# Kernel tuning notes

Measured on AMD Instinct MI355X. Metric: run time of the kernel, lower is better.

## Reference

```python
import jax, jax.numpy as jnp
import numpy as np

B, N, C = 8, 4096, 1024
H = 16
D = C // H  # head_dim = 64
SCALE = D ** -0.5


def setup_inputs() -> dict:
    key = jax.random.key(0)
    ks = jax.random.split(key, 5)
    std = C ** -0.5
    return {
        "x": jax.random.normal(ks[0], (B, N, C), dtype=jnp.float32),
        "Wq": jax.random.normal(ks[1], (C, C), dtype=jnp.float32) * std,
        "Wk": jax.random.normal(ks[2], (C, C), dtype=jnp.float32) * std,
        "Wv": jax.random.normal(ks[3], (C, C), dtype=jnp.float32) * std,
        "Wo": jax.random.normal(ks[4], (C, C), dtype=jnp.float32) * std,
        "bo": jnp.zeros((C,), dtype=jnp.float32),
    }


def reference(x, Wq, Wk, Wv, Wo, bo):
    b, n, c = x.shape
    # projections -> (B, N, H, D)
    q = (x @ Wq).reshape(b, n, H, D)
    k = (x @ Wk).reshape(b, n, H, D)
    v = (x @ Wv).reshape(b, n, H, D)
    # feature maps: softmax over head_dim for q, over sequence for k
    q = jax.nn.softmax(q, axis=-1) * SCALE
    k = jax.nn.softmax(k, axis=1)
    # O(N) linear attention: kv summary then apply to q
    kv = jnp.einsum("bnhf,bnhd->bhfd", k, v)   # (B, H, D, D)
    y = jnp.einsum("bnhf,bhfd->bnhd", q, kv)   # (B, N, H, D)
    y = y.reshape(b, n, H * D)
    return y @ Wo + bo
```

## Files before the change

kernel.cpp:

```cpp
#include <hip/hip_runtime.h>


typedef unsigned short u16;
typedef __bf16 bf16x8v __attribute__((ext_vector_type(8)));
typedef float f32x4 __attribute__((ext_vector_type(4)));
typedef u16 u16x8 __attribute__((ext_vector_type(8)));
typedef u16 u16x4 __attribute__((ext_vector_type(4)));

#define AS1C(p) (const __attribute__((address_space(1))) void*)(p)
#define AS3(p)  (__attribute__((address_space(3))) void*)(p)

__device__ __forceinline__ float b2f(u16 u) {
    union { unsigned u; float f; } c; c.u = ((unsigned)u) << 16; return c.f;
}
__device__ __forceinline__ u16 f2b(float f) {
    union { float f; unsigned u; } c; c.f = f;
    unsigned x = c.u + 0x7fffu + ((c.u >> 16) & 1u);
    return (u16)(x >> 16);
}

__global__ void cast_x_kernel(const float* __restrict__ in, u16* __restrict__ out, long n4) {
    long i = (long)blockIdx.x * blockDim.x + threadIdx.x;
    long stride = (long)gridDim.x * blockDim.x;
    for (long j = i; j < n4; j += stride) {
        float4 v = ((const float4*)in)[j];
        u16x4 o = { f2b(v.x), f2b(v.y), f2b(v.z), f2b(v.w) };
        ((u16x4*)out)[j] = o;
    }
}

__global__ void transpose_cast4(const float* __restrict__ Wq, const float* __restrict__ Wk,
                                const float* __restrict__ Wv, const float* __restrict__ Wo,
                                u16* __restrict__ wt, u16* __restrict__ wot) {
    __shared__ float tl[64][65];
    const int which = blockIdx.x >> 8;
    const float* src = which == 0 ? Wq : which == 1 ? Wk : which == 2 ? Wv : Wo;
    u16* dst = which < 3 ? wt + which * 1048576 : wot;
    const int bx = blockIdx.x & 255;
    const int tx = bx & 15, ty = bx >> 4;
    const int j = threadIdx.x & 63, i0 = threadIdx.x >> 6;
    #pragma unroll
    for (int it = 0; it < 16; ++it) {
        int i = it * 4 + i0;
        tl[i][j] = src[(ty * 64 + i) * 1024 + tx * 64 + j];
    }
    __syncthreads();
    #pragma unroll
    for (int it = 0; it < 16; ++it) {
        int i = it * 4 + i0;
        dst[(tx * 64 + i) * 1024 + ty * 64 + j] = f2b(tl[j][i]);
    }
}

template<int OUTMODE>
__global__ __launch_bounds__(512, 2) void gemm256(
    const u16* __restrict__ A, const u16* __restrict__ Bt,
    void* __restrict__ Cout, const float* __restrict__ bias,
    const int lda, const int ldc, const int ntn, const int nwg)
{
    __shared__ __align__(16) u16 lds[65536];
    const int t = threadIdx.x;
    const int w = t >> 6, lane = t & 63;
    const int l16 = lane & 15, g = lane >> 4;
    const int wr = w >> 2, wc = w & 3;

    const int cpx = nwg >> 3;
    const int bid = blockIdx.x;
    const int swzb = (bid & 7) * cpx + (bid >> 3);
    const int tm = swzb / ntn, tn = swzb - tm * ntn;
    const long row0 = (long)tm << 8, col0 = (long)tn << 8;

    const int rloc = (w << 3) + (lane >> 3);
    const int eo = (((lane & 7) ^ (lane >> 3)) << 3);
    const u16* pA = A + (row0 + rloc) * (long)lda + eo;
    const u16* pB = Bt + (col0 + rloc) * 1024L + eo;
    const long a64 = (long)lda << 6;
    const int wdst = w << 9;

#define STG_A(Tt, j) __builtin_amdgcn_global_load_lds(                        \
    AS1C(pA + (long)(j) * a64 + ((long)(Tt) << 6)),                           \
    AS3(lds + ((((Tt) & 1) << 15) + ((j) << 12) + wdst)), 16, 0, 0);
#define STG_B(Tt, j) __builtin_amdgcn_global_load_lds(                        \
    AS1C(pB + (long)(j) * 65536L + ((long)(Tt) << 6)),                        \
    AS3(lds + ((((Tt) & 1) << 15) + 16384 + ((j) << 12) + wdst)), 16, 0, 0);

    const int sw0 = ((g ^ (l16 & 7)) << 3);
    const int arB = ((wr << 7) + l16) * 64 + sw0;
    const int brB = 16384 + ((wc << 6) + l16) * 64 + sw0;

#define RD_A(m) { _Pragma("unroll") for (int mi = 0; mi < 4; ++mi) {          \
    const int ab = bufE + arB + (m) * 4096 + mi * 1024;                       \
    areg[mi][0] = *(const u16x8*)&lds[ab];                                    \
    areg[mi][1] = *(const u16x8*)&lds[ab ^ 32]; } }
#define RD_B(n, br) { _Pragma("unroll") for (int ni = 0; ni < 2; ++ni) {      \
    const int bb = bufE + brB + (n) * 2048 + ni * 1024;                       \
    br[ni][0] = *(const u16x8*)&lds[bb];                                      \
    br[ni][1] = *(const u16x8*)&lds[bb ^ 32]; } }
#define MM(mo, no, br) { _Pragma("unroll") for (int mi = 0; mi < 4; ++mi)     \
    { _Pragma("unroll") for (int ni = 0; ni < 2; ++ni) {                      \
    f32x4 c = acc[(mo) + mi][(no) + ni];                                      \
    c = __builtin_amdgcn_mfma_f32_16x16x32_bf16(                              \
        __builtin_bit_cast(bf16x8v, areg[mi][0]),                             \
        __builtin_bit_cast(bf16x8v, br[ni][0]), c, 0, 0, 0);                  \
    c = __builtin_amdgcn_mfma_f32_16x16x32_bf16(                              \
        __builtin_bit_cast(bf16x8v, areg[mi][1]),                             \
        __builtin_bit_cast(bf16x8v, br[ni][1]), c, 0, 0, 0);                  \
    acc[(mo) + mi][(no) + ni] = c; } } }
#define BAR { __builtin_amdgcn_s_barrier(); __builtin_amdgcn_sched_barrier(0); }

    u16x8 areg[4][2], breg0[2][2], breg1[2][2];
    f32x4 acc[8][4] = {};

    STG_A(0, 0) STG_A(0, 1) STG_A(0, 2) STG_A(0, 3)
    STG_B(0, 0) STG_B(0, 1) STG_B(0, 2) STG_B(0, 3)
    STG_A(1, 0) STG_A(1, 1) STG_A(1, 2) STG_A(1, 3)
    STG_B(1, 0) STG_B(1, 1) STG_B(1, 2) STG_B(1, 3)
    asm volatile("s_waitcnt vmcnt(8)" ::: "memory");
    __builtin_amdgcn_sched_barrier(0);
    BAR

    #pragma unroll 2
    for (int T = 0; T < 16; ++T) {
        const int bufE = (T & 1) << 15;
        const int Tp = T + 2;
        RD_A(0) RD_B(0, breg0)
        BAR
        __builtin_amdgcn_s_setprio(1); MM(0, 0, breg0) __builtin_amdgcn_s_setprio(0);
        BAR
        RD_B(1, breg1)
        STG_A(Tp, 0) STG_A(Tp, 2)
        BAR
        __builtin_amdgcn_s_setprio(1); MM(0, 2, breg1) __builtin_amdgcn_s_setprio(0);
        BAR
        RD_A(1)
        STG_B(Tp, 0) STG_B(Tp, 1)
        BAR
        __builtin_amdgcn_s_setprio(1); MM(4, 0, breg0) __builtin_amdgcn_s_setprio(0);
        BAR
        STG_A(Tp, 1) STG_A(Tp, 3)
        STG_B(Tp, 2) STG_B(Tp, 3)
        BAR
        __builtin_amdgcn_s_setprio(1); MM(4, 2, breg1) __builtin_amdgcn_s_setprio(0);
        asm volatile("s_waitcnt vmcnt(8)" ::: "memory");
        __builtin_amdgcn_sched_barrier(0);
        BAR
    }
    asm volatile("s_waitcnt vmcnt(0)" ::: "memory");
#undef STG_A
#undef STG_B
#undef RD_A
#undef RD_B
#undef MM
#undef BAR

    const long crow = row0 + wr * 128 + g * 4;
    const long ccol = col0 + wc * 64 + l16;
    if (OUTMODE == 0) {
        u16* Cb = (u16*)Cout;
        #pragma unroll
        for (int mi = 0; mi < 8; ++mi) {
            #pragma unroll
            for (int ni = 0; ni < 4; ++ni) {
                long base = (crow + mi * 16) * (long)ldc + ccol + ni * 16;
                #pragma unroll
                for (int r = 0; r < 4; ++r)
                    Cb[base + (long)r * ldc] = f2b(acc[mi][ni][r]);
            }
        }
    } else {
        float* Cf = (float*)Cout;
        float bv[4];
        #pragma unroll
        for (int ni = 0; ni < 4; ++ni) bv[ni] = bias[ccol + ni * 16];
        #pragma unroll
        for (int mi = 0; mi < 8; ++mi) {
            #pragma unroll
            for (int ni = 0; ni < 4; ++ni) {
                long base = (crow + mi * 16) * (long)ldc + ccol + ni * 16;
                #pragma unroll
                for (int r = 0; r < 4; ++r)
                    Cf[base + (long)r * ldc] = acc[mi][ni][r] + bv[ni];
            }
        }
    }
}

__global__ __launch_bounds__(256) void kv_partial(const u16* __restrict__ qkv,
                                                  float* __restrict__ kvp,
                                                  float* __restrict__ psum) {
    __shared__ __align__(16) float kf_s[64 * 68];
    __shared__ __align__(16) float v_s[64 * 68];
    const int t = threadIdx.x;
    const int bx = blockIdx.x;
    const int nc = bx & 7, h = (bx >> 3) & 15, b = bx >> 7;
    const int f0 = (t >> 4) << 2;
    const int d0 = (t & 15) << 2;
    const int lr = t >> 3, lc = (t & 7) << 3;
    const long rowbase = (long)b * 4096 + nc * 512;
    const u16* kfg = qkv + (rowbase + lr) * 3072 + 1024 + h * 64 + lc;
    const u16* vg = kfg + 1024;
    float acc[4][4] = {};
    float cs[4] = {};
    for (int n0 = 0; n0 < 512; n0 += 64) {
        long go = (long)n0 * 3072;
        u16x8 kr0 = *(const u16x8*)(kfg + go);
        u16x8 kr1 = *(const u16x8*)(kfg + go + 32L * 3072);
        u16x8 vr0 = *(const u16x8*)(vg + go);
        u16x8 vr1 = *(const u16x8*)(vg + go + 32L * 3072);
        f32x4 ke0a, ke0b, ke1a, ke1b, vv0a, vv0b, vv1a, vv1b;
        #pragma unroll
        for (int j = 0; j < 4; ++j) {
            ke0a[j] = __expf(b2f(kr0[j]));     ke0b[j] = __expf(b2f(kr0[j + 4]));
            ke1a[j] = __expf(b2f(kr1[j]));     ke1b[j] = __expf(b2f(kr1[j + 4]));
            vv0a[j] = b2f(vr0[j]);             vv0b[j] = b2f(vr0[j + 4]);
            vv1a[j] = b2f(vr1[j]);             vv1b[j] = b2f(vr1[j + 4]);
        }
        *(f32x4*)&kf_s[lr * 68 + lc]            = ke0a;
        *(f32x4*)&kf_s[lr * 68 + lc + 4]        = ke0b;
        *(f32x4*)&kf_s[(lr + 32) * 68 + lc]     = ke1a;
        *(f32x4*)&kf_s[(lr + 32) * 68 + lc + 4] = ke1b;
        *(f32x4*)&v_s[lr * 68 + lc]             = vv0a;
        *(f32x4*)&v_s[lr * 68 + lc + 4]         = vv0b;
        *(f32x4*)&v_s[(lr + 32) * 68 + lc]      = vv1a;
        *(f32x4*)&v_s[(lr + 32) * 68 + lc + 4]  = vv1b;
        __syncthreads();
        #pragma unroll 8
        for (int r = 0; r < 64; ++r) {
            f32x4 kf4 = *(const f32x4*)&kf_s[r * 68 + f0];
            f32x4 vf4 = *(const f32x4*)&v_s[r * 68 + d0];
            #pragma unroll
            for (int i = 0; i < 4; ++i) {
                cs[i] += kf4[i];
                #pragma unroll
                for (int jj = 0; jj < 4; ++jj)
                    acc[i][jj] += kf4[i] * vf4[jj];
            }
        }
        __syncthreads();
    }
    float* o = kvp + (long)nc * 524288 + ((long)(b * 16 + h)) * 4096;
    #pragma unroll
    for (int i = 0; i < 4; ++i) {
        #pragma unroll
        for (int jj = 0; jj < 4; ++jj)
            o[(f0 + i) * 64 + d0 + jj] = acc[i][jj];
    }
    if ((t & 15) == 0) {
        float* ps = psum + ((long)nc * 128 + b * 16 + h) * 64 + f0;
        #pragma unroll
        for (int i = 0; i < 4; ++i) ps[i] = cs[i];
    }
}

__global__ void kv_combine_T(const float* __restrict__ kvp, const float* __restrict__ psum,
                             u16* __restrict__ kvTb) {
    __shared__ float tl[64 * 65];
    __shared__ float inv_s[64];
    const int bh = blockIdx.x;
    const int t = threadIdx.x;
    if (t < 64) {
        float s = 0.f;
        #pragma unroll
        for (int nc = 0; nc < 8; ++nc) s += psum[((long)nc * 128 + bh) * 64 + t];
        inv_s[t] = 1.0f / s;
    }
    __syncthreads();
    const float* p = kvp + (long)bh * 4096;
    #pragma unroll
    for (int it = 0; it < 16; ++it) {
        int idx = it * 256 + t;
        float v = 0.f;
        #pragma unroll
        for (int nc = 0; nc < 8; ++nc) v += p[(long)nc * 524288 + idx];
        tl[(idx & 63) * 65 + (idx >> 6)] = v * inv_s[idx >> 6];
    }
    __syncthreads();
    u16* o = kvTb + (long)bh * 4096;
    #pragma unroll
    for (int it = 0; it < 16; ++it) {
        int idx = it * 256 + t;
        o[idx] = f2b(tl[(idx >> 6) * 65 + (idx & 63)]);
    }
}

__global__ __launch_bounds__(256) void apply_mfma(u16* __restrict__ qkv,
                                                  const u16* __restrict__ kvTb) {
    __shared__ __align__(16) u16 Qs[8192];
    const int t = threadIdx.x;
    const int bx = blockIdx.x;
    const int nt = bx & 31, h = (bx >> 5) & 15, b = bx >> 9;
    const long n0 = (long)b * 4096 + (long)nt * 128;
    const int wave = t >> 6, lane = t & 63;
    const int wr = wave >> 1, wc = wave & 1;
    const int l16 = lane & 15, g = lane >> 4;

    const int colg = t & 7;
    const int rloc = t >> 3;
    #pragma unroll
    for (int p = 0; p < 4; ++p) {
        const int row = p * 32 + rloc;
        u16x8 qv = *(const u16x8*)(qkv + (n0 + row) * 3072 + h * 64 + colg * 8);
        float f[8];
        #pragma unroll
        for (int j = 0; j < 8; ++j) f[j] = b2f(qv[j]);
        float m = f[0];
        #pragma unroll
        for (int j = 1; j < 8; ++j) m = fmaxf(m, f[j]);
        m = fmaxf(m, __shfl_xor(m, 1)); m = fmaxf(m, __shfl_xor(m, 2)); m = fmaxf(m, __shfl_xor(m, 4));
        float s = 0.f;
        #pragma unroll
        for (int j = 0; j < 8; ++j) { f[j] = __expf(f[j] - m); s += f[j]; }
        s += __shfl_xor(s, 1); s += __shfl_xor(s, 2); s += __shfl_xor(s, 4);
        const float sc = 0.125f / s;
        u16x8 ov;
        #pragma unroll
        for (int j = 0; j < 8; ++j) ov[j] = f2b(f[j] * sc);
        const int chunk = colg ^ (row & 7);
        *(u16x8*)&Qs[row * 64 + chunk * 8] = ov;
    }
    __syncthreads();

    const u16* kvb = kvTb + ((long)(b * 16 + h) << 12);
    bf16x8v bkv[2][2];
    #pragma unroll
    for (int ni = 0; ni < 2; ++ni) {
        #pragma unroll
        for (int ks = 0; ks < 2; ++ks)
            bkv[ni][ks] = __builtin_bit_cast(bf16x8v,
                *(const u16x8*)(kvb + (wc * 32 + ni * 16 + l16) * 64 + ks * 32 + g * 8));
    }
    bf16x8v aq[4][2];
    #pragma unroll
    for (int mi = 0; mi < 4; ++mi) {
        const int row = wr * 64 + mi * 16 + l16;
        #pragma unroll
        for (int ks = 0; ks < 2; ++ks) {
            const int c16 = (ks * 4 + g) ^ (row & 7);
            aq[mi][ks] = __builtin_bit_cast(bf16x8v,
                *(const u16x8*)&Qs[row * 64 + c16 * 8]);
        }
    }
    f32x4 acc[4][2] = {};
    #pragma unroll
    for (int mi = 0; mi < 4; ++mi) {
        #pragma unroll
        for (int ni = 0; ni < 2; ++ni) {
            acc[mi][ni] = __builtin_amdgcn_mfma_f32_16x16x32_bf16(
                aq[mi][0], bkv[ni][0], acc[mi][ni], 0, 0, 0);
            acc[mi][ni] = __builtin_amdgcn_mfma_f32_16x16x32_bf16(
                aq[mi][1], bkv[ni][1], acc[mi][ni], 0, 0, 0);
        }
    }
    #pragma unroll
    for (int mi = 0; mi < 4; ++mi) {
        #pragma unroll
        for (int ni = 0; ni < 2; ++ni) {
            long row = n0 + wr * 64 + mi * 16 + g * 4;
            int col = h * 64 + wc * 32 + ni * 16 + l16;
            #pragma unroll
            for (int r = 0; r < 4; ++r)
                qkv[(row + r) * 3072 + col] = f2b(acc[mi][ni][r]);
        }
    }
}

extern "C" void kernel_launch(void* const* d_in, const int* in_sizes, int n_in,
                              void* d_out, int out_size, void* d_ws, size_t ws_size,
                              hipStream_t stream) {
    (void)in_sizes; (void)n_in; (void)out_size; (void)ws_size;
    const float* x  = (const float*)d_in[0];
    const float* Wq = (const float*)d_in[1];
    const float* Wk = (const float*)d_in[2];
    const float* Wv = (const float*)d_in[3];
    const float* Wo = (const float*)d_in[4];
    const float* bo = (const float*)d_in[5];

    u16* xb  = (u16*)d_ws;
    u16* wt  = xb + 33554432;
    u16* wot = wt + 3145728;
    u16* qkv = wot + 1048576;
    u16*   kvTb = qkv + 100663296;
    float* kvp  = (float*)xb;
    float* psum = kvp + 4194304;

    cast_x_kernel<<<2048, 256, 0, stream>>>(x, xb, 8388608L);
    transpose_cast4<<<1024, 256, 0, stream>>>(Wq, Wk, Wv, Wo, wt, wot);
    gemm256<0><<<1536, 512, 0, stream>>>(xb, wt, (void*)qkv, nullptr, 1024, 3072, 12, 1536);
    kv_partial<<<1024, 256, 0, stream>>>(qkv, kvp, psum);
    kv_combine_T<<<128, 256, 0, stream>>>(kvp, psum, kvTb);
    apply_mfma<<<4096, 256, 0, stream>>>(qkv, kvTb);
    gemm256<1><<<512, 512, 0, stream>>>(qkv, wot, d_out, bo, 3072, 1024, 4, 512);
}
```

Baseline: 436.4 us.

## Switch GEMM to 32x32x16 MFMA with double-buffered register fragments and fewer barriers

Replaces the 16x16x32 bf16 MFMA tiling in the 256x256 GEMM with 32x32x16 MFMA tiles, remapping LDS fragment offsets and the output write indexing. The k-loop is restructured so LDS reads for the next k-slice are ping-ponged in two register sets while MFMAs run, and the per-iteration global-to-LDS staging is issued in one batch between two barriers instead of being interleaved across eight barriers. This aims to cut LDS read traffic per FLOP and barrier overhead. It risks exposing global load latency, since all staging now sits at one point in the iteration.

```diff
diff --git a/kernel.cpp b/kernel.cpp
--- a/kernel.cpp
+++ b/kernel.cpp
@@ -4,6 +4,7 @@
 typedef unsigned short u16;
 typedef __bf16 bf16x8v __attribute__((ext_vector_type(8)));
 typedef float f32x4 __attribute__((ext_vector_type(4)));
+typedef float f32x16 __attribute__((ext_vector_type(16)));
 typedef u16 u16x8 __attribute__((ext_vector_type(8)));
 typedef u16 u16x4 __attribute__((ext_vector_type(4)));
 
@@ -61,7 +62,7 @@
     __shared__ __align__(16) u16 lds[65536];
     const int t = threadIdx.x;
     const int w = t >> 6, lane = t & 63;
-    const int l16 = lane & 15, g = lane >> 4;
+    const int l31 = lane & 31, g2 = lane >> 5;
     const int wr = w >> 2, wc = w & 3;
 
     const int cpx = nwg >> 3;
@@ -84,32 +85,29 @@
     AS1C(pB + (long)(j) * 65536L + ((long)(Tt) << 6)),                        \
     AS3(lds + ((((Tt) & 1) << 15) + 16384 + ((j) << 12) + wdst)), 16, 0, 0);
 
-    const int sw0 = ((g ^ (l16 & 7)) << 3);
-    const int arB = ((wr << 7) + l16) * 64 + sw0;
-    const int brB = 16384 + ((wc << 6) + l16) * 64 + sw0;
-
-#define RD_A(m) { _Pragma("unroll") for (int mi = 0; mi < 4; ++mi) {          \
-    const int ab = bufE + arB + (m) * 4096 + mi * 1024;                       \
-    areg[mi][0] = *(const u16x8*)&lds[ab];                                    \
-    areg[mi][1] = *(const u16x8*)&lds[ab ^ 32]; } }
-#define RD_B(n, br) { _Pragma("unroll") for (int ni = 0; ni < 2; ++ni) {      \
-    const int bb = bufE + brB + (n) * 2048 + ni * 1024;                       \
-    br[ni][0] = *(const u16x8*)&lds[bb];                                      \
-    br[ni][1] = *(const u16x8*)&lds[bb ^ 32]; } }
-#define MM(mo, no, br) { _Pragma("unroll") for (int mi = 0; mi < 4; ++mi)     \
-    { _Pragma("unroll") for (int ni = 0; ni < 2; ++ni) {                      \
-    f32x4 c = acc[(mo) + mi][(no) + ni];                                      \
-    c = __builtin_amdgcn_mfma_f32_16x16x32_bf16(                              \
-        __builtin_bit_cast(bf16x8v, areg[mi][0]),                             \
-        __builtin_bit_cast(bf16x8v, br[ni][0]), c, 0, 0, 0);                  \
-    c = __builtin_amdgcn_mfma_f32_16x16x32_bf16(                              \
-        __builtin_bit_cast(bf16x8v, areg[mi][1]),                             \
-        __builtin_bit_cast(bf16x8v, br[ni][1]), c, 0, 0, 0);                  \
-    acc[(mo) + mi][(no) + ni] = c; } } }
-#define BAR { __builtin_amdgcn_s_barrier(); __builtin_amdgcn_sched_barrier(0); }
-
-    u16x8 areg[4][2], breg0[2][2], breg1[2][2];
-    f32x4 acc[8][4] = {};
+    const int swA = l31 & 7;
+    int aoff[4], boff[2], koff[4];
+    #pragma unroll
+    for (int mb = 0; mb < 4; ++mb) aoff[mb] = ((wr << 7) + (mb << 5) + l31) << 6;
+    #pragma unroll
+    for (int nb = 0; nb < 2; ++nb) boff[nb] = 16384 + (((wc << 6) + (nb << 5) + l31) << 6);
+    #pragma unroll
+    for (int s = 0; s < 4; ++s) koff[s] = (((s << 1) | g2) ^ swA) << 3;
+
+    u16x8 areg[2][4], breg[2][2];
+    f32x16 acc[4][2] = {};
+
+#define RDS(set, s, bufX) {                                                   \
+    _Pragma("unroll") for (int mb = 0; mb < 4; ++mb)                          \
+        areg[set][mb] = *(const u16x8*)&lds[(bufX) + aoff[mb] + koff[s]];     \
+    _Pragma("unroll") for (int nb = 0; nb < 2; ++nb)                          \
+        breg[set][nb] = *(const u16x8*)&lds[(bufX) + boff[nb] + koff[s]]; }
+#define MM(set) { _Pragma("unroll") for (int mb = 0; mb < 4; ++mb)            \
+    { _Pragma("unroll") for (int nb = 0; nb < 2; ++nb)                        \
+        acc[mb][nb] = __builtin_amdgcn_mfma_f32_32x32x16_bf16(                \
+            __builtin_bit_cast(bf16x8v, areg[set][mb]),                       \
+            __builtin_bit_cast(bf16x8v, breg[set][nb]),                       \
+            acc[mb][nb], 0, 0, 0); } }
 
     STG_A(0, 0) STG_A(0, 1) STG_A(0, 2) STG_A(0, 3)
     STG_B(0, 0) STG_B(0, 1) STG_B(0, 2) STG_B(0, 3)
@@ -117,69 +115,67 @@
     STG_B(1, 0) STG_B(1, 1) STG_B(1, 2) STG_B(1, 3)
     asm volatile("s_waitcnt vmcnt(8)" ::: "memory");
     __builtin_amdgcn_sched_barrier(0);
-    BAR
+    __builtin_amdgcn_s_barrier();
+    __builtin_amdgcn_sched_barrier(0);
+    RDS(0, 0, 0)
 
     #pragma unroll 2
     for (int T = 0; T < 16; ++T) {
         const int bufE = (T & 1) << 15;
+        const int bufN = bufE ^ 32768;
         const int Tp = T + 2;
-        RD_A(0) RD_B(0, breg0)
-        BAR
-        __builtin_amdgcn_s_setprio(1); MM(0, 0, breg0) __builtin_amdgcn_s_setprio(0);
-        BAR
-        RD_B(1, breg1)
-        STG_A(Tp, 0) STG_A(Tp, 2)
-        BAR
-        __builtin_amdgcn_s_setprio(1); MM(0, 2, breg1) __builtin_amdgcn_s_setprio(0);
-        BAR
-        RD_A(1)
-        STG_B(Tp, 0) STG_B(Tp, 1)
-        BAR
-        __builtin_amdgcn_s_setprio(1); MM(4, 0, breg0) __builtin_amdgcn_s_setprio(0);
-        BAR
-        STG_A(Tp, 1) STG_A(Tp, 3)
-        STG_B(Tp, 2) STG_B(Tp, 3)
-        BAR
-        __builtin_amdgcn_s_setprio(1); MM(4, 2, breg1) __builtin_amdgcn_s_setprio(0);
+        RDS(1, 1, bufE)
+        __builtin_amdgcn_s_setprio(1); MM(0) __builtin_amdgcn_s_setprio(0);
+        RDS(0, 2, bufE)
+        __builtin_amdgcn_s_setprio(1); MM(1) __builtin_amdgcn_s_setprio(0);
+        RDS(1, 3, bufE)
+        __builtin_amdgcn_s_setprio(1); MM(0) __builtin_amdgcn_s_setprio(0);
+        __builtin_amdgcn_s_setprio(1); MM(1) __builtin_amdgcn_s_setprio(0);
+        __builtin_amdgcn_s_barrier();
+        __builtin_amdgcn_sched_barrier(0);
+        STG_A(Tp, 0) STG_A(Tp, 1) STG_A(Tp, 2) STG_A(Tp, 3)
+        STG_B(Tp, 0) STG_B(Tp, 1) STG_B(Tp, 2) STG_B(Tp, 3)
         asm volatile("s_waitcnt vmcnt(8)" ::: "memory");
         __builtin_amdgcn_sched_barrier(0);
-        BAR
+        __builtin_amdgcn_s_barrier();
+        __builtin_amdgcn_sched_barrier(0);
+        RDS(0, 0, bufN)
     }
     asm volatile("s_waitcnt vmcnt(0)" ::: "memory");
 #undef STG_A
 #undef STG_B
-#undef RD_A
-#undef RD_B
+#undef RDS
 #undef MM
-#undef BAR
-
-    const long crow = row0 + wr * 128 + g * 4;
-    const long ccol = col0 + wc * 64 + l16;
+
+    const long crow0 = row0 + wr * 128 + g2 * 4;
+    const long ccol0 = col0 + wc * 64 + l31;
     if (OUTMODE == 0) {
         u16* Cb = (u16*)Cout;
         #pragma unroll
-        for (int mi = 0; mi < 8; ++mi) {
+        for (int mb = 0; mb < 4; ++mb) {
             #pragma unroll
-            for (int ni = 0; ni < 4; ++ni) {
-                long base = (crow + mi * 16) * (long)ldc + ccol + ni * 16;
+            for (int nb = 0; nb < 2; ++nb) {
                 #pragma unroll
-                for (int r = 0; r < 4; ++r)
-                    Cb[base + (long)r * ldc] = f2b(acc[mi][ni][r]);
+                for (int r = 0; r < 16; ++r) {
+                    long row = crow0 + mb * 32 + (r & 3) + ((r >> 2) << 3);
+                    Cb[row * (long)ldc + ccol0 + nb * 32] = f2b(acc[mb][nb][r]);
+                }
             }
         }
     } else {
         float* Cf = (float*)Cout;
-        float bv[4];
-        #pragma unroll
-        for (int ni = 0; ni < 4; ++ni) bv[ni] = bias[ccol + ni * 16];
-        #pragma unroll
-        for (int mi = 0; mi < 8; ++mi) {
+        float bv[2];
+        #pragma unroll
+        for (int nb = 0; nb < 2; ++nb) bv[nb] = bias[ccol0 + nb * 32];
+        #pragma unroll
+        for (int mb = 0; mb < 4; ++mb) {
             #pragma unroll
-            for (int ni = 0; ni < 4; ++ni) {
-                long base = (crow + mi * 16) * (long)ldc + ccol + ni * 16;
+            for (int nb = 0; nb < 2; ++nb) {
                 #pragma unroll
-                for (int r = 0; r < 4; ++r)
-                    Cf[base + (long)r * ldc] = acc[mi][ni][r] + bv[ni];
+                for (int r = 0; r < 16; ++r) {
+                    long row = crow0 + mb * 32 + (r & 3) + ((r >> 2) << 3);
+                    Cf[row * (long)ldc + ccol0 + nb * 32] = acc[mb][nb][r] + bv[nb];
+                }
             }
         }
     }
```

Result: slower. 474.8 us (+8.8%).
